# Performance work log

Hardware: AMD Instinct MI355X
Metric: run time of the kernel (lower is better)

The kernel has to match this reference:

```python
import jax, jax.numpy as jnp
import numpy as np

NUM_HEADS = 16

def setup_inputs() -> dict:
    key = jax.random.key(0)
    k1, k2, k3 = jax.random.split(key, 3)
    B, S, D = 4, 2048, 1024
    x = jax.random.normal(k1, (B, S, D), dtype=jnp.float32)
    w_qkv = jax.random.normal(k2, (D, 3 * D), dtype=jnp.float32) * (1.0 / np.sqrt(D))
    b_qkv = jnp.zeros((3 * D,), dtype=jnp.float32)
    w_out = jax.random.normal(k3, (D, D), dtype=jnp.float32) * (1.0 / np.sqrt(D))
    b_out = jnp.zeros((D,), dtype=jnp.float32)
    return {"x": x, "w_qkv": w_qkv, "b_qkv": b_qkv, "w_out": w_out, "b_out": b_out}

def reference(x, w_qkv, b_qkv, w_out, b_out):
    B, S, D = x.shape
    H = NUM_HEADS
    Dh = D // H
    # fused QKV projection: [B,S,3D]
    qkv = jnp.einsum('bsd,de->bse', x, w_qkv) + b_qkv
    q, k, v = jnp.split(qkv, 3, axis=-1)
    # separate heads -> [B,H,S,Dh]
    def heads(t):
        return t.reshape(B, S, H, Dh).transpose(0, 2, 1, 3)
    q, k, v = heads(q), heads(k), heads(v)
    # scaled dot-product attention (no mask, no dropout)
    scale = 1.0 / jnp.sqrt(jnp.asarray(Dh, dtype=x.dtype))
    attn = jnp.einsum('bhqd,bhkd->bhqk', q, k) * scale
    weights = jax.nn.softmax(attn, axis=-1)
    out = jnp.einsum('bhqk,bhkd->bhqd', weights, v)
    # combine heads -> [B,S,D], then output projection
    out = out.transpose(0, 2, 1, 3).reshape(B, S, D)
    return jnp.einsum('bsd,de->bse', out, w_out) + b_out
```

## Files before the change

### kernel.cpp

```cpp
#include <hip/hip_runtime.h>

typedef unsigned short u16;
typedef __attribute__((ext_vector_type(8))) short v8s;
typedef __attribute__((ext_vector_type(4))) short v4s;
typedef __attribute__((ext_vector_type(4))) float v4f;

#define MFMA16(a, b, c) __builtin_amdgcn_mfma_f32_16x16x32_bf16(a, b, c, 0, 0, 0)

static __device__ __forceinline__ u16 f32_to_bf16(float f) {
    unsigned int u = __builtin_bit_cast(unsigned int, f);
    u += 0x7fffu + ((u >> 16) & 1u);
    return (u16)(u >> 16);
}
static __device__ __forceinline__ v8s cvt8(v4f lo, v4f hi) {
    v8s r;
#pragma unroll
    for (int i = 0; i < 4; i++) {
        r[i]     = (short)f32_to_bf16(lo[i]);
        r[i + 4] = (short)f32_to_bf16(hi[i]);
    }
    return r;
}

__global__ void cast_f32_bf16(const float* __restrict__ in,
                              u16* __restrict__ out, int n8) {
    const int i = blockIdx.x * blockDim.x + threadIdx.x;
    if (i < n8) {
        v4f lo = ((const v4f*)in)[2 * i];
        v4f hi = ((const v4f*)in)[2 * i + 1];
        ((v8s*)out)[i] = cvt8(lo, hi);
    }
}

__global__ void transpose_f32_bf16(const float* __restrict__ in,
                                   u16* __restrict__ out, int R, int C) {
    __shared__ u16 t[32][33];
    const int tid = threadIdx.x;
    const int tx = tid & 31, ty = tid >> 5;
    const int c0 = blockIdx.x * 32, r0 = blockIdx.y * 32;
#pragma unroll
    for (int i = 0; i < 32; i += 8)
        t[ty + i][tx] = f32_to_bf16(in[(size_t)(r0 + ty + i) * C + c0 + tx]);
    __syncthreads();
#pragma unroll
    for (int i = 0; i < 32; i += 8)
        out[(size_t)(c0 + ty + i) * R + r0 + tx] = t[tx][ty + i];
}

template <int AMODE, int CMODE>
__global__ __launch_bounds__(256)
void gemm_bt(const void* __restrict__ A, int lda,
             const u16* __restrict__ Bt, int ldb,
             const float* __restrict__ bias,
             void* __restrict__ Cq, u16* __restrict__ Kb, u16* __restrict__ VtG,
             int ldc, int K) {
    __shared__ __align__(16) u16 As[128 * 72];
    __shared__ __align__(16) u16 Bs[128 * 72];

    const int tid  = threadIdx.x;
    const int wid  = tid >> 6;
    const int lane = tid & 63;
    const int l15  = lane & 15;
    const int quad = lane >> 4;
    const int bm = blockIdx.y * 128;
    const int bn = blockIdx.x * 128;
    const int wm = (wid & 1) * 64;
    const int wn = (wid >> 1) * 64;

    const int sr = tid >> 3;
    const int sg = (tid & 7) * 8;

    const float* Af = (const float*)A;
    const u16*   Au = (const u16*)A;

    v4f acc[4][4];
#pragma unroll
    for (int i = 0; i < 4; i++)
#pragma unroll
        for (int j = 0; j < 4; j++) acc[i][j] = (v4f)0.f;

    for (int kb = 0; kb < K; kb += 64) {
        v8s a[4], b[4];
#pragma unroll
        for (int i = 0; i < 4; i++) {
            const int row = sr + i * 32;
            if (AMODE) {
                const float* p = Af + (size_t)(bm + row) * lda + kb + sg;
                a[i] = cvt8(*(const v4f*)p, *(const v4f*)(p + 4));
            } else {
                a[i] = *(const v8s*)(Au + (size_t)(bm + row) * lda + kb + sg);
            }
            b[i] = *(const v8s*)(Bt + (size_t)(bn + row) * ldb + kb + sg);
        }
        __syncthreads();
#pragma unroll
        for (int i = 0; i < 4; i++) {
            const int row = sr + i * 32;
            *(v8s*)&As[row * 72 + sg] = a[i];
            *(v8s*)&Bs[row * 72 + sg] = b[i];
        }
        __syncthreads();

        v8s af[2][4], bf[2][4];
#pragma unroll
        for (int ko = 0; ko < 2; ko++) {
#pragma unroll
            for (int mt = 0; mt < 4; mt++)
                af[ko][mt] = *(const v8s*)&As[(wm + mt * 16 + l15) * 72 + ko * 32 + quad * 8];
#pragma unroll
            for (int nt = 0; nt < 4; nt++)
                bf[ko][nt] = *(const v8s*)&Bs[(wn + nt * 16 + l15) * 72 + ko * 32 + quad * 8];
        }
#pragma unroll
        for (int ko = 0; ko < 2; ko++)
#pragma unroll
            for (int mt = 0; mt < 4; mt++)
#pragma unroll
                for (int nt = 0; nt < 4; nt++)
                    acc[mt][nt] = MFMA16(af[ko][mt], bf[ko][nt], acc[mt][nt]);
    }

#pragma unroll
    for (int nt = 0; nt < 4; nt++) {
        const int n = bn + wn + nt * 16 + l15;
        const float bv = bias[n];
#pragma unroll
        for (int mt = 0; mt < 4; mt++) {
#pragma unroll
            for (int r = 0; r < 4; r++) {
                const int m = bm + wm + mt * 16 + quad * 4 + r;
                const float val = acc[mt][nt][r] + bv;
                if (CMODE == 1) {
                    ((float*)Cq)[(size_t)m * ldc + n] = val;
                } else {
                    const u16 o = f32_to_bf16(val);
                    const int region = n >> 10, nl = n & 1023;
                    if (region == 0) {
                        ((u16*)Cq)[(size_t)m * 1024 + nl] = o;
                    } else if (region == 1) {
                        Kb[(size_t)m * 1024 + nl] = o;
                    } else {
                        const int h = nl >> 6, dh = nl & 63;
                        const int b = m >> 11, s = m & 2047;
                        VtG[((size_t)((b * 16 + h) * 64 + dh)) * 2048 + s] = o;
                    }
                }
            }
        }
    }
}

__global__ __launch_bounds__(256)
void attn_fused(u16* __restrict__ Qb, const u16* __restrict__ Kb,
                const u16* __restrict__ VtG) {
    __shared__ __align__(16) u16 Ks[64 * 72];
    __shared__ __align__(16) u16 Vs[64 * 72];
    __shared__ __align__(16) u16 Ps[4 * 16 * 72];

    const int tid  = threadIdx.x;
    const int wid  = tid >> 6;
    const int lane = tid & 63;
    const int l15  = lane & 15;
    const int quad = lane >> 4;
    const int qt = blockIdx.x;
    const int h  = blockIdx.y;
    const int bz = blockIdx.z;

    const size_t qbase = (size_t)bz * 2048 * 1024;
    const int q0 = qt * 64 + wid * 16;
    const u16* qrow = Qb + qbase + (size_t)(q0 + l15) * 1024 + h * 64 + quad * 8;
    const v8s aq0 = *(const v8s*)qrow;
    const v8s aq1 = *(const v8s*)(qrow + 32);

    u16* psw = &Ps[wid * 16 * 72];
    float lrow = 0.f;
    v4f accO[4];
#pragma unroll
    for (int c = 0; c < 4; c++) accO[c] = (v4f)0.f;

    const int sr = tid >> 3;
    const int sg = (tid & 7) * 8;
    const float SC = 0.18033688f;

    const u16* kpb = Kb + qbase + h * 64;
    const u16* vpb = VtG + (size_t)((bz * 16 + h) * 64) * 2048;

    for (int kt = 0; kt < 32; kt++) {
        const v8s k0 = *(const v8s*)(kpb + (size_t)(kt * 64 + sr) * 1024 + sg);
        const v8s k1 = *(const v8s*)(kpb + (size_t)(kt * 64 + sr + 32) * 1024 + sg);
        const v8s v0 = *(const v8s*)(vpb + (size_t)sr * 2048 + kt * 64 + sg);
        const v8s v1 = *(const v8s*)(vpb + (size_t)(sr + 32) * 2048 + kt * 64 + sg);
        __syncthreads();
        *(v8s*)&Ks[sr * 72 + sg]        = k0;
        *(v8s*)&Ks[(sr + 32) * 72 + sg] = k1;
        *(v8s*)&Vs[sr * 72 + sg]        = v0;
        *(v8s*)&Vs[(sr + 32) * 72 + sg] = v1;
        __syncthreads();

#pragma unroll
        for (int kc = 0; kc < 4; kc++) {
            const v8s kf0 = *(const v8s*)&Ks[(kc * 16 + l15) * 72 + quad * 8];
            const v8s kf1 = *(const v8s*)&Ks[(kc * 16 + l15) * 72 + 32 + quad * 8];
            v4f st = (v4f)0.f;
            st = MFMA16(kf0, aq0, st);
            st = MFMA16(kf1, aq1, st);
            v4s pk;
            float rs = 0.f;
#pragma unroll
            for (int r = 0; r < 4; r++) {
                const float p = exp2f(st[r] * SC);
                rs += p;
                pk[r] = (short)f32_to_bf16(p);
            }
            lrow += rs;
            *(v4s*)&psw[l15 * 72 + kc * 16 + quad * 4] = pk;
        }
        __threadfence_block();

        const v8s ap0 = *(const v8s*)&psw[l15 * 72 + quad * 8];
        const v8s ap1 = *(const v8s*)&psw[l15 * 72 + 32 + quad * 8];
#pragma unroll
        for (int c = 0; c < 4; c++) {
            const v8s bv0 = *(const v8s*)&Vs[(c * 16 + l15) * 72 + quad * 8];
            const v8s bv1 = *(const v8s*)&Vs[(c * 16 + l15) * 72 + 32 + quad * 8];
            accO[c] = MFMA16(ap0, bv0, accO[c]);
            accO[c] = MFMA16(ap1, bv1, accO[c]);
        }
    }

    lrow += __shfl_xor(lrow, 16);
    lrow += __shfl_xor(lrow, 32);
    float lq[4];
#pragma unroll
    for (int r = 0; r < 4; r++) lq[r] = __shfl(lrow, quad * 4 + r);

#pragma unroll
    for (int c = 0; c < 4; c++) {
#pragma unroll
        for (int r = 0; r < 4; r++) {
            const int q = q0 + quad * 4 + r;
            Qb[qbase + (size_t)q * 1024 + h * 64 + c * 16 + l15] =
                f32_to_bf16(accO[c][r] / lq[r]);
        }
    }
}

extern "C" void kernel_launch(void* const* d_in, const int* in_sizes, int n_in,
                              void* d_out, int out_size, void* d_ws, size_t ws_size,
                              hipStream_t stream) {
    (void)in_sizes; (void)n_in; (void)out_size;
    const float* x    = (const float*)d_in[0];
    const float* wqkv = (const float*)d_in[1];
    const float* bqkv = (const float*)d_in[2];
    const float* wout = (const float*)d_in[3];
    const float* bout = (const float*)d_in[4];
    float* outp = (float*)d_out;

    char* ws = (char*)d_ws;
    const size_t BIG  = 58720256;
    const size_t BIGX = 75497472;

    if (ws_size >= BIG || ws_size == 0) {
        u16* Qb    = (u16*)(ws);
        u16* Kb    = (u16*)(ws + 16777216);
        u16* VtG   = (u16*)(ws + 33554432);
        u16* wqkvT = (u16*)(ws + 50331648);
        u16* woutT = (u16*)(ws + 56623104);
        u16* xb    = (u16*)(ws + 58720256);

        transpose_f32_bf16<<<dim3(96, 32), 256, 0, stream>>>(wqkv, wqkvT, 1024, 3072);
        transpose_f32_bf16<<<dim3(32, 32), 256, 0, stream>>>(wout, woutT, 1024, 1024);
        if (ws_size >= BIGX) {
            cast_f32_bf16<<<4096, 256, 0, stream>>>(x, xb, 1048576);
            gemm_bt<0, 2><<<dim3(24, 64), 256, 0, stream>>>(
                xb, 1024, wqkvT, 1024, bqkv, Qb, Kb, VtG, 0, 1024);
        } else {
            gemm_bt<1, 2><<<dim3(24, 64), 256, 0, stream>>>(
                x, 1024, wqkvT, 1024, bqkv, Qb, Kb, VtG, 0, 1024);
        }
        attn_fused<<<dim3(32, 16, 4), 256, 0, stream>>>(Qb, Kb, VtG);
        gemm_bt<0, 1><<<dim3(8, 64), 256, 0, stream>>>(
            Qb, 1024, woutT, 1024, bout, outp, nullptr, nullptr, 1024, 1024);
    } else {
        u16* wqkvT = (u16*)(ws);
        u16* woutT = (u16*)(ws + 6291456);
        u16* Qb    = (u16*)(ws + 8388608);
        u16* Kb    = (u16*)(ws + 12582912);
        u16* VtG   = (u16*)(ws + 16777216);

        transpose_f32_bf16<<<dim3(96, 32), 256, 0, stream>>>(wqkv, wqkvT, 1024, 3072);
        transpose_f32_bf16<<<dim3(32, 32), 256, 0, stream>>>(wout, woutT, 1024, 1024);
        for (int b = 0; b < 4; b++) {
            const float* xb = x + (size_t)b * 2048 * 1024;
            float* ob = outp + (size_t)b * 2048 * 1024;
            gemm_bt<1, 2><<<dim3(24, 16), 256, 0, stream>>>(
                xb, 1024, wqkvT, 1024, bqkv, Qb, Kb, VtG, 0, 1024);
            attn_fused<<<dim3(32, 16, 1), 256, 0, stream>>>(Qb, Kb, VtG);
            gemm_bt<0, 1><<<dim3(8, 16), 256, 0, stream>>>(
                Qb, 1024, woutT, 1024, bout, ob, nullptr, nullptr, 1024, 1024);
        }
    }
}
```

Baseline: 363.7 us.

## Keep attention probabilities in registers and process two query tiles per wave

The attention kernel drops the shared-memory staging of the probability tile. The S^T MFMA output layout is fed directly as the B operand of a 16x16x16 MFMA against V, which removes the LDS write/read round trip. Each wave now handles 32 query rows instead of 16, so every K/V tile loaded into LDS is reused twice and the grid is halved. In exchange, the PV product uses the smaller-K MFMA (or a zero-padded fallback), register pressure goes up, and fewer blocks are launched.

```diff
diff --git a/kernel.cpp b/kernel.cpp
--- a/kernel.cpp
+++ b/kernel.cpp
@@ -5,7 +5,20 @@
 typedef __attribute__((ext_vector_type(4))) short v4s;
 typedef __attribute__((ext_vector_type(4))) float v4f;
 
-#define MFMA16(a, b, c) __builtin_amdgcn_mfma_f32_16x16x32_bf16(a, b, c, 0, 0, 0)
+#define MFMA32(a, b, c) __builtin_amdgcn_mfma_f32_16x16x32_bf16(a, b, c, 0, 0, 0)
+
+#if __has_builtin(__builtin_amdgcn_mfma_f32_16x16x16bf16_1k)
+static __device__ __forceinline__ v4f mfma16(v4s a, v4s b, v4f c) {
+    return __builtin_amdgcn_mfma_f32_16x16x16bf16_1k(a, b, c, 0, 0, 0);
+}
+#else
+static __device__ __forceinline__ v4f mfma16(v4s a, v4s b, v4f c) {
+    v4s z = {0, 0, 0, 0};
+    v8s a8 = __builtin_shufflevector(a, z, 0, 1, 2, 3, 4, 5, 6, 7);
+    v8s b8 = __builtin_shufflevector(b, z, 0, 1, 2, 3, 4, 5, 6, 7);
+    return MFMA32(a8, b8, c);
+}
+#endif
 
 static __device__ __forceinline__ u16 f32_to_bf16(float f) {
     unsigned int u = __builtin_bit_cast(unsigned int, f);
@@ -117,7 +130,7 @@
             for (int mt = 0; mt < 4; mt++)
 #pragma unroll
                 for (int nt = 0; nt < 4; nt++)
-                    acc[mt][nt] = MFMA16(af[ko][mt], bf[ko][nt], acc[mt][nt]);
+                    acc[mt][nt] = MFMA32(af[ko][mt], bf[ko][nt], acc[mt][nt]);
     }
 
 #pragma unroll
@@ -155,7 +168,6 @@
                 const u16* __restrict__ VtG) {
     __shared__ __align__(16) u16 Ks[64 * 72];
     __shared__ __align__(16) u16 Vs[64 * 72];
-    __shared__ __align__(16) u16 Ps[4 * 16 * 72];
 
     const int tid  = threadIdx.x;
     const int wid  = tid >> 6;
@@ -167,16 +179,22 @@
     const int bz = blockIdx.z;
 
     const size_t qbase = (size_t)bz * 2048 * 1024;
-    const int q0 = qt * 64 + wid * 16;
-    const u16* qrow = Qb + qbase + (size_t)(q0 + l15) * 1024 + h * 64 + quad * 8;
-    const v8s aq0 = *(const v8s*)qrow;
-    const v8s aq1 = *(const v8s*)(qrow + 32);
-
-    u16* psw = &Ps[wid * 16 * 72];
-    float lrow = 0.f;
-    v4f accO[4];
-#pragma unroll
-    for (int c = 0; c < 4; c++) accO[c] = (v4f)0.f;
+    const int q0 = qt * 128 + wid * 32;
+
+    v8s aq[2][2];
+#pragma unroll
+    for (int qh = 0; qh < 2; qh++) {
+        const u16* qrow = Qb + qbase + (size_t)(q0 + qh * 16 + l15) * 1024 + h * 64 + quad * 8;
+        aq[qh][0] = *(const v8s*)qrow;
+        aq[qh][1] = *(const v8s*)(qrow + 32);
+    }
+
+    float lrow[2] = {0.f, 0.f};
+    v4f accO[2][4];
+#pragma unroll
+    for (int qh = 0; qh < 2; qh++)
+#pragma unroll
+        for (int c = 0; c < 4; c++) accO[qh][c] = (v4f)0.f;
 
     const int sr = tid >> 3;
     const int sg = (tid & 7) * 8;
@@ -201,46 +219,49 @@
         for (int kc = 0; kc < 4; kc++) {
             const v8s kf0 = *(const v8s*)&Ks[(kc * 16 + l15) * 72 + quad * 8];
             const v8s kf1 = *(const v8s*)&Ks[(kc * 16 + l15) * 72 + 32 + quad * 8];
-            v4f st = (v4f)0.f;
-            st = MFMA16(kf0, aq0, st);
-            st = MFMA16(kf1, aq1, st);
-            v4s pk;
-            float rs = 0.f;
-#pragma unroll
-            for (int r = 0; r < 4; r++) {
-                const float p = exp2f(st[r] * SC);
-                rs += p;
-                pk[r] = (short)f32_to_bf16(p);
+            v4s vf[4];
+#pragma unroll
+            for (int c = 0; c < 4; c++)
+                vf[c] = *(const v4s*)&Vs[(c * 16 + l15) * 72 + kc * 16 + quad * 4];
+
+#pragma unroll
+            for (int qh = 0; qh < 2; qh++) {
+                v4f st = (v4f)0.f;
+                st = MFMA32(kf0, aq[qh][0], st);
+                st = MFMA32(kf1, aq[qh][1], st);
+                v4s pk;
+                float rs = 0.f;
+#pragma unroll
+                for (int r = 0; r < 4; r++) {
+                    const float p = exp2f(st[r] * SC);
+                    rs += p;
+                    pk[r] = (short)f32_to_bf16(p);
+                }
+                lrow[qh] += rs;
+#pragma unroll
+                for (int c = 0; c < 4; c++)
+                    accO[qh][c] = mfma16(vf[c], pk, accO[qh][c]);
             }
-            lrow += rs;
-            *(v4s*)&psw[l15 * 72 + kc * 16 + quad * 4] = pk;
-        }
-        __threadfence_block();
-
-        const v8s ap0 = *(const v8s*)&psw[l15 * 72 + quad * 8];
-        const v8s ap1 = *(const v8s*)&psw[l15 * 72 + 32 + quad * 8];
+        }
+    }
+
+#pragma unroll
+    for (int qh = 0; qh < 2; qh++) {
+        lrow[qh] += __shfl_xor(lrow[qh], 16);
+        lrow[qh] += __shfl_xor(lrow[qh], 32);
+    }
+
+#pragma unroll
+    for (int qh = 0; qh < 2; qh++) {
+        const int q = q0 + qh * 16 + l15;
+        const float inv = 1.f / lrow[qh];
 #pragma unroll
         for (int c = 0; c < 4; c++) {
-            const v8s bv0 = *(const v8s*)&Vs[(c * 16 + l15) * 72 + quad * 8];
-            const v8s bv1 = *(const v8s*)&Vs[(c * 16 + l15) * 72 + 32 + quad * 8];
-            accO[c] = MFMA16(ap0, bv0, accO[c]);
-            accO[c] = MFMA16(ap1, bv1, accO[c]);
-        }
-    }
-
-    lrow += __shfl_xor(lrow, 16);
-    lrow += __shfl_xor(lrow, 32);
-    float lq[4];
-#pragma unroll
-    for (int r = 0; r < 4; r++) lq[r] = __shfl(lrow, quad * 4 + r);
-
-#pragma unroll
-    for (int c = 0; c < 4; c++) {
-#pragma unroll
-        for (int r = 0; r < 4; r++) {
-            const int q = q0 + quad * 4 + r;
-            Qb[qbase + (size_t)q * 1024 + h * 64 + c * 16 + l15] =
-                f32_to_bf16(accO[c][r] / lq[r]);
+            v4s o;
+#pragma unroll
+            for (int r = 0; r < 4; r++)
+                o[r] = (short)f32_to_bf16(accO[qh][c][r] * inv);
+            *(v4s*)&Qb[qbase + (size_t)q * 1024 + h * 64 + c * 16 + quad * 4] = o;
         }
     }
 }
@@ -278,7 +299,7 @@
             gemm_bt<1, 2><<<dim3(24, 64), 256, 0, stream>>>(
                 x, 1024, wqkvT, 1024, bqkv, Qb, Kb, VtG, 0, 1024);
         }
-        attn_fused<<<dim3(32, 16, 4), 256, 0, stream>>>(Qb, Kb, VtG);
+        attn_fused<<<dim3(16, 16, 4), 256, 0, stream>>>(Qb, Kb, VtG);
         gemm_bt<0, 1><<<dim3(8, 64), 256, 0, stream>>>(
             Qb, 1024, woutT, 1024, bout, outp, nullptr, nullptr, 1024, 1024);
     } else {
@@ -295,7 +316,7 @@
             float* ob = outp + (size_t)b * 2048 * 1024;
             gemm_bt<1, 2><<<dim3(24, 16), 256, 0, stream>>>(
                 xb, 1024, wqkvT, 1024, bqkv, Qb, Kb, VtG, 0, 1024);
-            attn_fused<<<dim3(32, 16, 1), 256, 0, stream>>>(Qb, Kb, VtG);
+            attn_fused<<<dim3(16, 16, 1), 256, 0, stream>>>(Qb, Kb, VtG);
             gemm_bt<0, 1><<<dim3(8, 16), 256, 0, stream>>>(
                 Qb, 1024, woutT, 1024, bout, ob, nullptr, nullptr, 1024, 1024);
         }
```

After: 347.7 us. 1.05x faster.
